# Kernel tuning notes

Hardware: AMD Instinct MI355X
Metric: run time of the kernel (lower is better)

The kernel has to match this reference:

```python
import jax, jax.numpy as jnp
import numpy as np

H, W = 48, 48
L = H * W            # 2304 tokens
D = 256              # d_model
NH = 8               # heads (self and memory attn)
FF = 1024            # dim_feedforward
T = 2                # memory frames
BS = 1
GN_GROUPS = 32       # GNActDWConv2d default groups


def layernorm(x, g, b, eps=1e-5):
    m = jnp.mean(x, -1, keepdims=True)
    v = jnp.mean((x - m) ** 2, -1, keepdims=True)
    return (x - m) * jax.lax.rsqrt(v + eps) * g + b


def linear(x, Wt, b):
    # torch nn.Linear convention: Wt is [out, in]
    return x @ Wt.T + b


def mha_core(Q, K, V, nhead):
    # Q [Lq, bs, C], K/V [Lk, bs, C]; AOT MultiheadAttention core (eval: no dropout)
    Lq, bs, C = Q.shape
    hd = C // nhead
    Qh = (Q / np.float32(np.sqrt(hd))).reshape(Lq, bs, nhead, hd).transpose(1, 2, 0, 3)
    Kh = K.reshape(-1, bs, nhead, hd).transpose(1, 2, 0, 3)
    Vh = V.reshape(-1, bs, nhead, hd).transpose(1, 2, 0, 3)
    attn = jax.nn.softmax(jnp.einsum('bhqd,bhkd->bhqk', Qh, Kh), axis=-1)
    out = jnp.einsum('bhqk,bhkd->bhqd', attn, Vh)
    return out.transpose(2, 0, 1, 3).reshape(Lq, bs, C)


def groupnorm(x, g, b, groups, eps=1e-5):
    bs, c, h, w = x.shape
    xg = x.reshape(bs, groups, c // groups, h, w)
    m = jnp.mean(xg, (2, 3, 4), keepdims=True)
    v = jnp.mean((xg - m) ** 2, (2, 3, 4), keepdims=True)
    xg = (xg - m) * jax.lax.rsqrt(v + eps)
    return xg.reshape(bs, c, h, w) * g[None, :, None, None] + b[None, :, None, None]


def dwconv5(x, k):
    # depthwise 5x5, padding=2; x [bs,c,h,w], k [c,1,5,5]
    return jax.lax.conv_general_dilated(x, k, (1, 1), ((2, 2), (2, 2)),
                                        feature_group_count=x.shape[1])


def setup_inputs() -> dict:
    key = jax.random.key(0)
    ks = jax.random.split(key, 16)
    rn = lambda i, shape, s=1.0: jax.random.normal(ks[i], shape, jnp.float32) * s
    w = 0.02
    inp = {
        'tgt': rn(0, (L, BS, D)),
        'global_K': rn(1, (T, L, BS, D)),
        'global_V': rn(2, (T, L, BS, D)),
        'local_K': rn(3, (L, BS, D)),
        'local_V': rn(4, (L, BS, D)),
        # LayerNorms
        'ln1_g': jnp.ones(D, jnp.float32), 'ln1_b': jnp.zeros(D, jnp.float32),
        'ln2_g': jnp.ones(D, jnp.float32), 'ln2_b': jnp.zeros(D, jnp.float32),
        'ln3_g': jnp.ones(D, jnp.float32), 'ln3_b': jnp.zeros(D, jnp.float32),
        'ln4_g': jnp.ones(D, jnp.float32), 'ln4_b': jnp.zeros(D, jnp.float32),
        # self_attn (use_linear=True) Q/K/V + projection
        'sa_Wq': rn(5, (D, D), w), 'sa_bq': jnp.zeros(D, jnp.float32),
        'sa_Wk': rn(6, (D, D), w), 'sa_bk': jnp.zeros(D, jnp.float32),
        'sa_Wv': rn(7, (D, D), w), 'sa_bv': jnp.zeros(D, jnp.float32),
        'sa_Wo': rn(8, (D, D), w), 'sa_bo': jnp.zeros(D, jnp.float32),
        # block linear_Q
        'Wq': rn(9, (D, D), w), 'bq': jnp.zeros(D, jnp.float32),
        # long/short term attn projections (use_linear=False)
        'lt_Wo': rn(10, (D, D), w), 'lt_bo': jnp.zeros(D, jnp.float32),
        'st_Wo': rn(11, (D, D), w), 'st_bo': jnp.zeros(D, jnp.float32),
        # FFN: linear1 -> GN+GELU+DWConv -> linear2
        'W1': rn(12, (FF, D), w), 'b1': jnp.zeros(FF, jnp.float32),
        'gn_g': jnp.ones(FF, jnp.float32), 'gn_b': jnp.zeros(FF, jnp.float32),
        'dw_k': rn(13, (FF, 1, 5, 5), 0.05),
        'W2': rn(14, (D, FF), w), 'b2': jnp.zeros(D, jnp.float32),
    }
    return inp


def reference(tgt, global_K, global_V, local_K, local_V,
              ln1_g, ln1_b, ln2_g, ln2_b, ln3_g, ln3_b, ln4_g, ln4_b,
              sa_Wq, sa_bq, sa_Wk, sa_bk, sa_Wv, sa_bv, sa_Wo, sa_bo,
              Wq, bq, lt_Wo, lt_bo, st_Wo, st_bo,
              W1, b1, gn_g, gn_b, dw_k, W2, b2):
    # --- stage 1: self-attention ---
    _tgt = layernorm(tgt, ln1_g, ln1_b)
    q = linear(_tgt, sa_Wq, sa_bq)
    k = linear(_tgt, sa_Wk, sa_bk)
    v = linear(_tgt, sa_Wv, sa_bv)
    tgt2 = linear(mha_core(q, k, v, NH), sa_Wo, sa_bo)
    tgt = tgt + tgt2  # droppath is identity at eval

    # --- stage 2: long-term + short-term memory cross-attention ---
    _tgt = layernorm(tgt, ln2_g, ln2_b)
    curr_Q = linear(_tgt, Wq, bq)
    curr_K = curr_Q
    curr_V = _tgt

    flat_K = global_K.reshape(-1, BS, D)  # [T*L, bs, D]
    flat_V = global_V.reshape(-1, BS, D)
    tgt2 = linear(mha_core(curr_Q, flat_K, flat_V, NH), lt_Wo, lt_bo)

    k_st = layernorm(local_K + curr_K, ln4_g, ln4_b)
    v_st = layernorm(local_V + curr_V, ln4_g, ln4_b)
    tgt3 = linear(mha_core(curr_Q, k_st, v_st, NH), st_Wo, st_bo)

    tgt = tgt + tgt2 + tgt3

    # --- stage 3: FFN with GN + GELU + depthwise conv ---
    _tgt = layernorm(tgt, ln3_g, ln3_b)
    x = linear(_tgt, W1, b1)                        # [L, bs, FF]
    x = x.reshape(H, W, BS, FF).transpose(2, 3, 0, 1)  # [bs, FF, H, W]
    x = jax.nn.gelu(groupnorm(x, gn_g, gn_b, GN_GROUPS), approximate=False)
    x = dwconv5(x, dw_k)
    x = x.reshape(BS, FF, L).transpose(2, 0, 1)     # [L, bs, FF]
    tgt2 = linear(x, W2, b2)
    return tgt + tgt2
```

## Files before the change

kernel.cpp:

```cpp
#include <hip/hip_runtime.h>
#include <hip/hip_bf16.h>

#define L   2304
#define D   256
#define NHD 8
#define HD  32
#define FF  1024
#define HH  48
#define WWW 48
#define SPL 4
#define RCH 24
#define RP  (L / RCH)

typedef unsigned short bfraw;
typedef __attribute__((ext_vector_type(8))) short s8v;
typedef __attribute__((ext_vector_type(4))) float f4v;

__device__ __forceinline__ bfraw f2b(float x) {
    __hip_bfloat16 h = __float2bfloat16(x);
    return __builtin_bit_cast(bfraw, h);
}

__global__ __launch_bounds__(256) void diag_kernel(float* __restrict__ out, float c, int n)
{
    int i = blockIdx.x * 256 + threadIdx.x;
    if (i < n) out[i] = c;
}

__global__ __launch_bounds__(256) void ln_kernel(
    const float* __restrict__ inA, const float* __restrict__ inB,
    const float* __restrict__ g, const float* __restrict__ b,
    float* __restrict__ out, bfraw* __restrict__ outb)
{
    int row = blockIdx.x, t = threadIdx.x;
    size_t idx = (size_t)row * D + t;
    float v = inA[idx];
    if (inB) v += inB[idx];
    __shared__ float rs[256], rq[256];
    rs[t] = v; rq[t] = v * v;
    __syncthreads();
    for (int o = 128; o > 0; o >>= 1) {
        if (t < o) { rs[t] += rs[t + o]; rq[t] += rq[t + o]; }
        __syncthreads();
    }
    float mean = rs[0] * (1.f / D);
    float var  = rq[0] * (1.f / D) - mean * mean;
    float rstd = rsqrtf(var + 1e-5f);
    float r = (v - mean) * rstd * g[t] + b[t];
    out[idx] = r;
    if (outb) outb[idx] = f2b(r);
}

__global__ __launch_bounds__(256) void gemm_mfma(
    const float* __restrict__ A, const float* __restrict__ W,
    const float* __restrict__ bias, const float* res, float* out,
    bfraw* __restrict__ outb,
    int M, int N, int K)
{
    __shared__ __attribute__((aligned(16))) short Al[32][32];
    __shared__ __attribute__((aligned(16))) short Wl[64][32];
    int t = threadIdx.x;
    int w = t >> 6, l = t & 63;
    int lo = l & 15, quad = l >> 4;
    int m0 = blockIdx.x * 32, n0 = blockIdx.y * 64;
    int wr = (w & 1) * 16, wc = (w >> 1) * 32;
    f4v acc[2];
    acc[0] = (f4v){0.f, 0.f, 0.f, 0.f};
    acc[1] = (f4v){0.f, 0.f, 0.f, 0.f};

    int aswz = (quad ^ ((lo >> 2) & 3)) * 8;
    int arow = t >> 3, apart = t & 7;
    int acol = ((apart >> 1) ^ ((arow >> 2) & 3)) * 8 + (apart & 1) * 4;

    for (int k0 = 0; k0 < K; k0 += 32) {
        float4 a4 = *reinterpret_cast<const float4*>(A + (size_t)(m0 + arow) * K + k0 + apart * 4);
        float4 w4[2];
        #pragma unroll
        for (int i = 0; i < 2; i++) {
            int row = i * 32 + arow;
            w4[i] = *reinterpret_cast<const float4*>(W + (size_t)(n0 + row) * K + k0 + apart * 4);
        }
        __syncthreads();
        {
            ushort4 ab;
            ab.x = f2b(a4.x); ab.y = f2b(a4.y); ab.z = f2b(a4.z); ab.w = f2b(a4.w);
            *reinterpret_cast<ushort4*>(&Al[arow][acol]) = ab;
            #pragma unroll
            for (int i = 0; i < 2; i++) {
                int row = i * 32 + arow;
                int col = ((apart >> 1) ^ ((row >> 2) & 3)) * 8 + (apart & 1) * 4;
                ushort4 wb;
                wb.x = f2b(w4[i].x); wb.y = f2b(w4[i].y); wb.z = f2b(w4[i].z); wb.w = f2b(w4[i].w);
                *reinterpret_cast<ushort4*>(&Wl[row][col]) = wb;
            }
        }
        __syncthreads();
        s8v af = *reinterpret_cast<const s8v*>(&Al[wr + lo][aswz]);
        #pragma unroll
        for (int j = 0; j < 2; j++) {
            s8v wf = *reinterpret_cast<const s8v*>(&Wl[wc + j * 16 + lo][aswz]);
            acc[j] = __builtin_amdgcn_mfma_f32_16x16x32_bf16(af, wf, acc[j], 0, 0, 0);
        }
    }

    #pragma unroll
    for (int j = 0; j < 2; j++) {
        #pragma unroll
        for (int r = 0; r < 4; r++) {
            int mrow = m0 + wr + quad * 4 + r;
            int ncol = n0 + wc + j * 16 + lo;
            float v = acc[j][r] + bias[ncol];
            size_t idx = (size_t)mrow * N + ncol;
            if (res) v += res[idx];
            out[idx] = v;
            if (outb) outb[idx] = f2b(v);
        }
    }
}

__global__ __launch_bounds__(256) void cvt_kernel(
    const float* __restrict__ in, bfraw* __restrict__ out)
{
    size_t i = ((size_t)blockIdx.x * 256 + threadIdx.x) * 4;
    float4 v = *reinterpret_cast<const float4*>(in + i);
    ushort4 o;
    o.x = f2b(v.x); o.y = f2b(v.y); o.z = f2b(v.z); o.w = f2b(v.w);
    *reinterpret_cast<ushort4*>(out + i) = o;
}

__global__ __launch_bounds__(256) void cvtT_kernel(
    const float* __restrict__ in, bfraw* __restrict__ out, int N)
{
    __shared__ float Ls[32][33];
    int h = blockIdx.y, n0 = blockIdx.x * 32, t = threadIdx.x;
    int nl = t >> 3, dq = t & 7;
    float4 v = *reinterpret_cast<const float4*>(in + (size_t)(n0 + nl) * D + h * HD + dq * 4);
    Ls[nl][dq*4+0] = v.x; Ls[nl][dq*4+1] = v.y;
    Ls[nl][dq*4+2] = v.z; Ls[nl][dq*4+3] = v.w;
    __syncthreads();
    int dl = t >> 3, nq = t & 7;
    ushort4 o;
    o.x = f2b(Ls[nq*4+0][dl]); o.y = f2b(Ls[nq*4+1][dl]);
    o.z = f2b(Ls[nq*4+2][dl]); o.w = f2b(Ls[nq*4+3][dl]);
    *reinterpret_cast<ushort4*>(out + (size_t)(h * HD + dl) * N + n0 + nq * 4) = o;
}

__global__ __launch_bounds__(256) void attn_mfma_split(
    const bfraw* __restrict__ Qb, const bfraw* __restrict__ Kb,
    const bfraw* __restrict__ Vt, float* __restrict__ OP,
    float* __restrict__ ML, int Lk, int chunk, float scale)
{
    __shared__ __attribute__((aligned(16))) short Ks[64][32];
    __shared__ __attribute__((aligned(16))) short Vts[32][72];
    __shared__ __attribute__((aligned(16))) short Ps[4][16][72];
    int t = threadIdx.x;
    int w = t >> 6, l = t & 63;
    int h = blockIdx.y, q0 = blockIdx.x * 64 + w * 16, z = blockIdx.z;
    int lo = l & 15, quad = l >> 4;
    int kb = z * chunk, ke = kb + chunk;

    s8v qf = *reinterpret_cast<const s8v*>(Qb + (size_t)(q0 + lo) * D + h * HD + quad * 8);
    int kswz = (quad ^ ((lo >> 2) & 3)) * 8;

    int skey = t >> 2, spart = t & 3;
    int kcol = (spart ^ ((skey >> 2) & 3)) * 8;
    int sd = t >> 3, svp = t & 7;
    const bfraw* kp = Kb + (size_t)skey * D + h * HD + spart * 8;
    const bfraw* vp = Vt + (size_t)(h * HD + sd) * Lk + svp * 8;

    float m_r = -1e30f, l_r = 0.f;
    f4v o0 = {0.f, 0.f, 0.f, 0.f}, o1 = {0.f, 0.f, 0.f, 0.f};

    for (int k0 = kb; k0 < ke; k0 += 64) {
        s8v kv = *reinterpret_cast<const s8v*>(kp + (size_t)k0 * D);
        s8v vv = *reinterpret_cast<const s8v*>(vp + k0);
        __syncthreads();
        *reinterpret_cast<s8v*>(&Ks[skey][kcol]) = kv;
        *reinterpret_cast<s8v*>(&Vts[sd][svp * 8]) = vv;
        __syncthreads();

        f4v sc4[4];
        #pragma unroll
        for (int s = 0; s < 4; s++) {
            s8v kf = *reinterpret_cast<const s8v*>(&Ks[lo + 16 * s][kswz]);
            sc4[s] = __builtin_amdgcn_mfma_f32_16x16x32_bf16(kf, qf, (f4v){0.f,0.f,0.f,0.f}, 0, 0, 0);
        }
        float cm = -1e30f;
        #pragma unroll
        for (int s = 0; s < 4; s++)
            #pragma unroll
            for (int r = 0; r < 4; r++) {
                sc4[s][r] *= scale;
                cm = fmaxf(cm, sc4[s][r]);
            }
        cm = fmaxf(cm, __shfl_xor(cm, 16));
        cm = fmaxf(cm, __shfl_xor(cm, 32));
        float mnew = fmaxf(m_r, cm);
        float alpha = __expf(m_r - mnew);
        float ls = 0.f;
        #pragma unroll
        for (int s = 0; s < 4; s++) {
            float p0 = __expf(sc4[s][0] - mnew), p1 = __expf(sc4[s][1] - mnew);
            float p2 = __expf(sc4[s][2] - mnew), p3 = __expf(sc4[s][3] - mnew);
            ls += p0 + p1 + p2 + p3;
            ushort4 pk;
            pk.x = f2b(p0); pk.y = f2b(p1); pk.z = f2b(p2); pk.w = f2b(p3);
            *reinterpret_cast<ushort4*>(&Ps[w][lo][s * 16 + quad * 4]) = pk;
        }
        ls += __shfl_xor(ls, 16);
        ls += __shfl_xor(ls, 32);
        l_r = l_r * alpha + ls;
        m_r = mnew;
        #pragma unroll
        for (int r = 0; r < 4; r++) {
            float a = __shfl(alpha, quad * 4 + r);
            o0[r] *= a; o1[r] *= a;
        }
        #pragma unroll
        for (int kc = 0; kc < 2; kc++) {
            s8v pf = *reinterpret_cast<const s8v*>(&Ps[w][lo][kc * 32 + quad * 8]);
            s8v v0 = *reinterpret_cast<const s8v*>(&Vts[lo][kc * 32 + quad * 8]);
            s8v v1 = *reinterpret_cast<const s8v*>(&Vts[16 + lo][kc * 32 + quad * 8]);
            o0 = __builtin_amdgcn_mfma_f32_16x16x32_bf16(pf, v0, o0, 0, 0, 0);
            o1 = __builtin_amdgcn_mfma_f32_16x16x32_bf16(pf, v1, o1, 0, 0, 0);
        }
    }

    float* Oz = OP + (size_t)z * L * D;
    #pragma unroll
    for (int r = 0; r < 4; r++) {
        int qg = q0 + quad * 4 + r;
        Oz[(size_t)qg * D + h * HD + lo]      = o0[r];
        Oz[(size_t)qg * D + h * HD + 16 + lo] = o1[r];
    }
    if (l < 16) {
        size_t mi = (((size_t)z * NHD + h) * L + q0 + lo) * 2;
        ML[mi]     = m_r;
        ML[mi + 1] = l_r;
    }
}

__global__ __launch_bounds__(256) void attn_combine(
    const float* __restrict__ OP, const float* __restrict__ ML,
    float* __restrict__ O)
{
    int q = blockIdx.x, t = threadIdx.x, h = t >> 5;
    float m[SPL], lv[SPL];
    float M = -1e30f;
    #pragma unroll
    for (int s = 0; s < SPL; s++) {
        size_t mi = (((size_t)s * NHD + h) * L + q) * 2;
        m[s]  = ML[mi];
        lv[s] = ML[mi + 1];
        M = fmaxf(M, m[s]);
    }
    float wl = 0.f, acc = 0.f;
    #pragma unroll
    for (int s = 0; s < SPL; s++) {
        float w = __expf(m[s] - M);
        wl  += w * lv[s];
        acc += w * OP[(size_t)s * L * D + (size_t)q * D + t];
    }
    O[(size_t)q * D + t] = acc / wl;
}

__global__ __launch_bounds__(256) void gn_stats_part(
    const float* __restrict__ X, float* __restrict__ ps)
{
    int g = blockIdx.x, rc = blockIdx.y, t = threadIdx.x;
    int cq = (t & 7) * 4;
    int rl = t >> 3;
    int r0 = rc * RP;
    float s = 0.f, sq = 0.f;
    #pragma unroll
    for (int p = 0; p < RP / 32; p++) {
        int l = r0 + p * 32 + rl;
        float4 v = *reinterpret_cast<const float4*>(X + (size_t)l * FF + g * 32 + cq);
        s  += v.x + v.y + v.z + v.w;
        sq += v.x*v.x + v.y*v.y + v.z*v.z + v.w*v.w;
    }
    __shared__ float rs[256], rq[256];
    rs[t] = s; rq[t] = sq;
    __syncthreads();
    for (int o = 128; o > 0; o >>= 1) {
        if (t < o) { rs[t] += rs[t + o]; rq[t] += rq[t + o]; }
        __syncthreads();
    }
    if (t == 0) {
        ps[(g * RCH + rc) * 2]     = rs[0];
        ps[(g * RCH + rc) * 2 + 1] = rq[0];
    }
}

__global__ __launch_bounds__(64) void gn_stats_final(
    const float* __restrict__ ps, float* __restrict__ st)
{
    int g = threadIdx.x;
    if (g < 32) {
        float s = 0.f, sq = 0.f;
        for (int i = 0; i < RCH; i++) {
            s  += ps[(g * RCH + i) * 2];
            sq += ps[(g * RCH + i) * 2 + 1];
        }
        float n = (float)(L * 32);
        float mean = s / n;
        float var  = sq / n - mean * mean;
        st[g * 2]     = mean;
        st[g * 2 + 1] = rsqrtf(var + 1e-5f);
    }
}

__global__ __launch_bounds__(256) void gn_gelu_dwconv(
    const float* __restrict__ X, const float* __restrict__ st,
    const float* __restrict__ gg, const float* __restrict__ gb,
    const float* __restrict__ Kw, float* __restrict__ Y)
{
    __shared__ float tile[144][64];
    int h0 = blockIdx.x * 8, w0 = blockIdx.y * 8, c0 = blockIdx.z * 64;
    int t = threadIdx.x;
    int c = t & 63;
    int cg = (c0 + c) >> 5;
    float mu = st[2 * cg], rs = st[2 * cg + 1];
    float ga = gg[c0 + c], be = gb[c0 + c];

    for (int i = t; i < 144 * 64; i += 256) {
        int sp = i >> 6;
        int hy = h0 + (sp / 12) - 2, wx = w0 + (sp % 12) - 2;
        float v = 0.f;
        if (hy >= 0 && hy < HH && wx >= 0 && wx < WWW) {
            float x = X[(size_t)(hy * WWW + wx) * FF + c0 + c];
            x = (x - mu) * rs * ga + be;
            v = 0.5f * x * (1.f + erff(x * 0.70710678118654752f));
        }
        tile[sp][c] = v;
    }
    float kw[25];
    #pragma unroll
    for (int i = 0; i < 25; i++) kw[i] = Kw[(size_t)(c0 + c) * 25 + i];
    __syncthreads();

    int sgrp = t >> 6;
    for (int s = 0; s < 16; s++) {
        int sp = sgrp * 16 + s;
        int oh = sp >> 3, ow = sp & 7;
        float acc = 0.f;
        #pragma unroll
        for (int ky = 0; ky < 5; ky++)
            #pragma unroll
            for (int kx = 0; kx < 5; kx++)
                acc += tile[(oh + ky) * 12 + ow + kx][c] * kw[ky * 5 + kx];
        Y[(size_t)((h0 + oh) * WWW + w0 + ow) * FF + c0 + c] = acc;
    }
}

extern "C" void kernel_launch(void* const* d_in, const int* in_sizes, int n_in,
                              void* d_out, int out_size, void* d_ws, size_t ws_size,
                              hipStream_t stream)
{
    (void)in_sizes;
    float* out = (float*)d_out;

    if (n_in != 34) {
        diag_kernel<<<(out_size + 255) / 256, 256, 0, stream>>>(out, 2000.f, out_size);
        return;
    }

    const float* tgt    = (const float*)d_in[0];
    const float* gK     = (const float*)d_in[1];
    const float* gV     = (const float*)d_in[2];
    const float* lK     = (const float*)d_in[3];
    const float* lV     = (const float*)d_in[4];
    const float* ln1_g  = (const float*)d_in[5];
    const float* ln1_b  = (const float*)d_in[6];
    const float* ln2_g  = (const float*)d_in[7];
    const float* ln2_b  = (const float*)d_in[8];
    const float* ln3_g  = (const float*)d_in[9];
    const float* ln3_b  = (const float*)d_in[10];
    const float* ln4_g  = (const float*)d_in[11];
    const float* ln4_b  = (const float*)d_in[12];
    const float* sa_Wq  = (const float*)d_in[13];
    const float* sa_bq  = (const float*)d_in[14];
    const float* sa_Wk  = (const float*)d_in[15];
    const float* sa_bk  = (const float*)d_in[16];
    const float* sa_Wv  = (const float*)d_in[17];
    const float* sa_bv  = (const float*)d_in[18];
    const float* sa_Wo  = (const float*)d_in[19];
    const float* sa_bo  = (const float*)d_in[20];
    const float* Wq     = (const float*)d_in[21];
    const float* bq     = (const float*)d_in[22];
    const float* lt_Wo  = (const float*)d_in[23];
    const float* lt_bo  = (const float*)d_in[24];
    const float* st_Wo  = (const float*)d_in[25];
    const float* st_bo  = (const float*)d_in[26];
    const float* W1w    = (const float*)d_in[27];
    const float* b1w    = (const float*)d_in[28];
    const float* gn_g   = (const float*)d_in[29];
    const float* gn_b   = (const float*)d_in[30];
    const float* dw_k   = (const float*)d_in[31];
    const float* W2w    = (const float*)d_in[32];
    const float* b2w    = (const float*)d_in[33];

    const size_t LD = (size_t)L * D;
    const size_t NEED = (6 * LD + (size_t)L * FF + 64) * 4;
    float* ws = (float*)d_ws;
    float* t0 = ws + 0 * LD;
    float* t1 = ws + 1 * LD;
    float* t2 = ws + 2 * LD;
    float* t3 = ws + 3 * LD;
    float* t4 = ws + 4 * LD;
    float* t5 = ws + 5 * LD;
    float* X1 = t0;
    float* X2 = ws + 6 * LD;
    float* ST = X2 + (size_t)L * FF;
    bfraw* qb   = (bfraw*)X2;
    bfraw* kb1  = qb + LD;
    bfraw* vtb1 = qb + 3 * LD;
    bfraw* kb2  = qb + 5 * LD;
    bfraw* vtb2 = qb + 6 * LD;
    float* OP   = ws;
    float* ML   = X2 + (7 * LD) / 2;
    float* PS   = ML;

    if (ws_size < NEED) {
        int wsMiB = (int)(ws_size >> 20); if (wsMiB > 63) wsMiB = 63;
        diag_kernel<<<(out_size + 255) / 256, 256, 0, stream>>>(out, 64.f + (float)wsMiB, out_size);
        return;
    }

    const float scale = 0.17677669529663687f;
    dim3 gDD(L / 32, D / 64);
    dim3 gDF(L / 32, FF / 64);
    dim3 gATS(L / 64, NHD, SPL);
    int  cvtLD  = (int)(LD / 1024);
    dim3 gT1(L / 32, NHD);
    dim3 gT2(2 * L / 32, NHD);
    dim3 gGN(32, RCH);
    dim3 gDW(6, 6, 16);

    ln_kernel<<<L, 256, 0, stream>>>(tgt, nullptr, ln1_g, ln1_b, t0, nullptr);
    gemm_mfma<<<gDD, 256, 0, stream>>>(t0, sa_Wq, sa_bq, nullptr, t1, qb,  L, D, D);
    gemm_mfma<<<gDD, 256, 0, stream>>>(t0, sa_Wk, sa_bk, nullptr, t2, kb2, L, D, D);
    gemm_mfma<<<gDD, 256, 0, stream>>>(t0, sa_Wv, sa_bv, nullptr, t3, nullptr, L, D, D);
    cvtT_kernel<<<gT1, 256, 0, stream>>>(t3, vtb2, L);
    attn_mfma_split<<<gATS, 256, 0, stream>>>(qb, kb2, vtb2, OP, ML, L, L / SPL, scale);
    attn_combine<<<L, 256, 0, stream>>>(OP, ML, t4);
    gemm_mfma<<<gDD, 256, 0, stream>>>(t4, sa_Wo, sa_bo, tgt, t5, nullptr, L, D, D);

    ln_kernel<<<L, 256, 0, stream>>>(t5, nullptr, ln2_g, ln2_b, t0, nullptr);
    gemm_mfma<<<gDD, 256, 0, stream>>>(t0, Wq, bq, nullptr, t1, qb, L, D, D);
    ln_kernel<<<L, 256, 0, stream>>>(t1, lK, ln4_g, ln4_b, t2, kb2);
    ln_kernel<<<L, 256, 0, stream>>>(t0, lV, ln4_g, ln4_b, t3, nullptr);
    cvtT_kernel<<<gT1, 256, 0, stream>>>(t3, vtb2, L);
    cvt_kernel<<<2 * cvtLD, 256, 0, stream>>>(gK, kb1);
    cvtT_kernel<<<gT2, 256, 0, stream>>>(gV, vtb1, 2 * L);
    attn_mfma_split<<<gATS, 256, 0, stream>>>(qb, kb1, vtb1, OP, ML, 2 * L, 2 * L / SPL, scale);
    attn_combine<<<L, 256, 0, stream>>>(OP, ML, t4);
    gemm_mfma<<<gDD, 256, 0, stream>>>(t4, lt_Wo, lt_bo, t5, t5, nullptr, L, D, D);
    attn_mfma_split<<<gATS, 256, 0, stream>>>(qb, kb2, vtb2, OP, ML, L, L / SPL, scale);
    attn_combine<<<L, 256, 0, stream>>>(OP, ML, t4);
    gemm_mfma<<<gDD, 256, 0, stream>>>(t4, st_Wo, st_bo, t5, t5, nullptr, L, D, D);

    ln_kernel<<<L, 256, 0, stream>>>(t5, nullptr, ln3_g, ln3_b, t4, nullptr);
    gemm_mfma<<<gDF, 256, 0, stream>>>(t4, W1w, b1w, nullptr, X1, nullptr, L, FF, D);
    gn_stats_part<<<gGN, 256, 0, stream>>>(X1, PS);
    gn_stats_final<<<1, 64, 0, stream>>>(PS, ST);
    gn_gelu_dwconv<<<gDW, 256, 0, stream>>>(X1, ST, gn_g, gn_b, dw_k, X2);
    gemm_mfma<<<gDD, 256, 0, stream>>>(X2, W2w, b2w, t5, out, nullptr, L, D, FF);
}
```

Before: 363.4 us.

## Fold softmax scale into Q, use exp2 with lazy rescale, transpose PV output

The attention scale times log2(e) is folded into the bf16 Q written by the projection GEMM, so the attention kernel uses exp2 directly and skips the per-score multiply. The running max is only rescaled when any lane's new block max exceeds the old one by more than 8, which removes most alpha rescaling and shuffles. The PV MFMA operands are swapped and the output is staged through LDS to emit coalesced float4 stores. Lazy rescaling bounds growth at 2^8 per block, so there is some fp32 accumulation range risk. The stage-2 Q stays unscaled in fp32 for the K LayerNorm input, so only the bf16 copy carries the scale.

```diff
diff --git a/kernel.cpp b/kernel.cpp
--- a/kernel.cpp
+++ b/kernel.cpp
@@ -11,6 +11,7 @@
 #define SPL 4
 #define RCH 24
 #define RP  (L / RCH)
+#define S2LOG 0.25503486f
 
 typedef unsigned short bfraw;
 typedef __attribute__((ext_vector_type(8))) short s8v;
@@ -54,7 +55,7 @@
 __global__ __launch_bounds__(256) void gemm_mfma(
     const float* __restrict__ A, const float* __restrict__ W,
     const float* __restrict__ bias, const float* res, float* out,
-    bfraw* __restrict__ outb,
+    bfraw* __restrict__ outb, float oscale,
     int M, int N, int K)
 {
     __shared__ __attribute__((aligned(16))) short Al[32][32];
@@ -113,7 +114,7 @@
             size_t idx = (size_t)mrow * N + ncol;
             if (res) v += res[idx];
             out[idx] = v;
-            if (outb) outb[idx] = f2b(v);
+            if (outb) outb[idx] = f2b(v * oscale);
         }
     }
 }
@@ -148,11 +149,12 @@
 __global__ __launch_bounds__(256) void attn_mfma_split(
     const bfraw* __restrict__ Qb, const bfraw* __restrict__ Kb,
     const bfraw* __restrict__ Vt, float* __restrict__ OP,
-    float* __restrict__ ML, int Lk, int chunk, float scale)
+    float* __restrict__ ML, int Lk, int chunk)
 {
     __shared__ __attribute__((aligned(16))) short Ks[64][32];
     __shared__ __attribute__((aligned(16))) short Vts[32][72];
     __shared__ __attribute__((aligned(16))) short Ps[4][16][72];
+    __shared__ float Tb[4][16][33];
     int t = threadIdx.x;
     int w = t >> 6, l = t & 63;
     int h = blockIdx.y, q0 = blockIdx.x * 64 + w * 16, z = blockIdx.z;
@@ -189,19 +191,26 @@
         #pragma unroll
         for (int s = 0; s < 4; s++)
             #pragma unroll
-            for (int r = 0; r < 4; r++) {
-                sc4[s][r] *= scale;
+            for (int r = 0; r < 4; r++)
                 cm = fmaxf(cm, sc4[s][r]);
-            }
         cm = fmaxf(cm, __shfl_xor(cm, 16));
         cm = fmaxf(cm, __shfl_xor(cm, 32));
-        float mnew = fmaxf(m_r, cm);
-        float alpha = __expf(m_r - mnew);
+        bool skip = __all(cm <= m_r + 8.f);
+        if (!skip) {
+            float mnew = fmaxf(m_r, cm);
+            float alpha = __builtin_amdgcn_exp2f(m_r - mnew);
+            l_r *= alpha;
+            #pragma unroll
+            for (int r = 0; r < 4; r++) { o0[r] *= alpha; o1[r] *= alpha; }
+            m_r = mnew;
+        }
         float ls = 0.f;
         #pragma unroll
         for (int s = 0; s < 4; s++) {
-            float p0 = __expf(sc4[s][0] - mnew), p1 = __expf(sc4[s][1] - mnew);
-            float p2 = __expf(sc4[s][2] - mnew), p3 = __expf(sc4[s][3] - mnew);
+            float p0 = __builtin_amdgcn_exp2f(sc4[s][0] - m_r);
+            float p1 = __builtin_amdgcn_exp2f(sc4[s][1] - m_r);
+            float p2 = __builtin_amdgcn_exp2f(sc4[s][2] - m_r);
+            float p3 = __builtin_amdgcn_exp2f(sc4[s][3] - m_r);
             ls += p0 + p1 + p2 + p3;
             ushort4 pk;
             pk.x = f2b(p0); pk.y = f2b(p1); pk.z = f2b(p2); pk.w = f2b(p3);
@@ -209,30 +218,31 @@
         }
         ls += __shfl_xor(ls, 16);
         ls += __shfl_xor(ls, 32);
-        l_r = l_r * alpha + ls;
-        m_r = mnew;
-        #pragma unroll
-        for (int r = 0; r < 4; r++) {
-            float a = __shfl(alpha, quad * 4 + r);
-            o0[r] *= a; o1[r] *= a;
-        }
+        l_r += ls;
         #pragma unroll
         for (int kc = 0; kc < 2; kc++) {
             s8v pf = *reinterpret_cast<const s8v*>(&Ps[w][lo][kc * 32 + quad * 8]);
             s8v v0 = *reinterpret_cast<const s8v*>(&Vts[lo][kc * 32 + quad * 8]);
             s8v v1 = *reinterpret_cast<const s8v*>(&Vts[16 + lo][kc * 32 + quad * 8]);
-            o0 = __builtin_amdgcn_mfma_f32_16x16x32_bf16(pf, v0, o0, 0, 0, 0);
-            o1 = __builtin_amdgcn_mfma_f32_16x16x32_bf16(pf, v1, o1, 0, 0, 0);
-        }
-    }
-
+            o0 = __builtin_amdgcn_mfma_f32_16x16x32_bf16(v0, pf, o0, 0, 0, 0);
+            o1 = __builtin_amdgcn_mfma_f32_16x16x32_bf16(v1, pf, o1, 0, 0, 0);
+        }
+    }
+
+    #pragma unroll
+    for (int r = 0; r < 4; r++) {
+        Tb[w][lo][quad * 4 + r]      = o0[r];
+        Tb[w][lo][16 + quad * 4 + r] = o1[r];
+    }
     float* Oz = OP + (size_t)z * L * D;
-    #pragma unroll
-    for (int r = 0; r < 4; r++) {
-        int qg = q0 + quad * 4 + r;
-        Oz[(size_t)qg * D + h * HD + lo]      = o0[r];
-        Oz[(size_t)qg * D + h * HD + 16 + lo] = o1[r];
-    }
+    int ql = l >> 2, dq = (l & 3) * 8;
+    float4 u0, u1;
+    u0.x = Tb[w][ql][dq + 0]; u0.y = Tb[w][ql][dq + 1];
+    u0.z = Tb[w][ql][dq + 2]; u0.w = Tb[w][ql][dq + 3];
+    u1.x = Tb[w][ql][dq + 4]; u1.y = Tb[w][ql][dq + 5];
+    u1.z = Tb[w][ql][dq + 6]; u1.w = Tb[w][ql][dq + 7];
+    *reinterpret_cast<float4*>(Oz + (size_t)(q0 + ql) * D + h * HD + dq)     = u0;
+    *reinterpret_cast<float4*>(Oz + (size_t)(q0 + ql) * D + h * HD + dq + 4) = u1;
     if (l < 16) {
         size_t mi = (((size_t)z * NHD + h) * L + q0 + lo) * 2;
         ML[mi]     = m_r;
@@ -257,7 +267,7 @@
     float wl = 0.f, acc = 0.f;
     #pragma unroll
     for (int s = 0; s < SPL; s++) {
-        float w = __expf(m[s] - M);
+        float w = __builtin_amdgcn_exp2f(m[s] - M);
         wl  += w * lv[s];
         acc += w * OP[(size_t)s * L * D + (size_t)q * D + t];
     }
@@ -427,7 +437,6 @@
         return;
     }
 
-    const float scale = 0.17677669529663687f;
     dim3 gDD(L / 32, D / 64);
     dim3 gDF(L / 32, FF / 64);
     dim3 gATS(L / 64, NHD, SPL);
@@ -438,32 +447,32 @@
     dim3 gDW(6, 6, 16);
 
     ln_kernel<<<L, 256, 0, stream>>>(tgt, nullptr, ln1_g, ln1_b, t0, nullptr);
-    gemm_mfma<<<gDD, 256, 0, stream>>>(t0, sa_Wq, sa_bq, nullptr, t1, qb,  L, D, D);
-    gemm_mfma<<<gDD, 256, 0, stream>>>(t0, sa_Wk, sa_bk, nullptr, t2, kb2, L, D, D);
-    gemm_mfma<<<gDD, 256, 0, stream>>>(t0, sa_Wv, sa_bv, nullptr, t3, nullptr, L, D, D);
+    gemm_mfma<<<gDD, 256, 0, stream>>>(t0, sa_Wq, sa_bq, nullptr, t1, qb,  S2LOG, L, D, D);
+    gemm_mfma<<<gDD, 256, 0, stream>>>(t0, sa_Wk, sa_bk, nullptr, t2, kb2, 1.f,   L, D, D);
+    gemm_mfma<<<gDD, 256, 0, stream>>>(t0, sa_Wv, sa_bv, nullptr, t3, nullptr, 1.f, L, D, D);
     cvtT_kernel<<<gT1, 256, 0, stream>>>(t3, vtb2, L);
-    attn_mfma_split<<<gATS, 256, 0, stream>>>(qb, kb2, vtb2, OP, ML, L, L / SPL, scale);
+    attn_mfma_split<<<gATS, 256, 0, stream>>>(qb, kb2, vtb2, OP, ML, L, L / SPL);
     attn_combine<<<L, 256, 0, stream>>>(OP, ML, t4);
-    gemm_mfma<<<gDD, 256, 0, stream>>>(t4, sa_Wo, sa_bo, tgt, t5, nullptr, L, D, D);
+    gemm_mfma<<<gDD, 256, 0, stream>>>(t4, sa_Wo, sa_bo, tgt, t5, nullptr, 1.f, L, D, D);
 
     ln_kernel<<<L, 256, 0, stream>>>(t5, nullptr, ln2_g, ln2_b, t0, nullptr);
-    gemm_mfma<<<gDD, 256, 0, stream>>>(t0, Wq, bq, nullptr, t1, qb, L, D, D);
+    gemm_mfma<<<gDD, 256, 0, stream>>>(t0, Wq, bq, nullptr, t1, qb, S2LOG, L, D, D);
     ln_kernel<<<L, 256, 0, stream>>>(t1, lK, ln4_g, ln4_b, t2, kb2);
     ln_kernel<<<L, 256, 0, stream>>>(t0, lV, ln4_g, ln4_b, t3, nullptr);
     cvtT_kernel<<<gT1, 256, 0, stream>>>(t3, vtb2, L);
     cvt_kernel<<<2 * cvtLD, 256, 0, stream>>>(gK, kb1);
     cvtT_kernel<<<gT2, 256, 0, stream>>>(gV, vtb1, 2 * L);
-    attn_mfma_split<<<gATS, 256, 0, stream>>>(qb, kb1, vtb1, OP, ML, 2 * L, 2 * L / SPL, scale);
+    attn_mfma_split<<<gATS, 256, 0, stream>>>(qb, kb1, vtb1, OP, ML, 2 * L, 2 * L / SPL);
     attn_combine<<<L, 256, 0, stream>>>(OP, ML, t4);
-    gemm_mfma<<<gDD, 256, 0, stream>>>(t4, lt_Wo, lt_bo, t5, t5, nullptr, L, D, D);
-    attn_mfma_split<<<gATS, 256, 0, stream>>>(qb, kb2, vtb2, OP, ML, L, L / SPL, scale);
+    gemm_mfma<<<gDD, 256, 0, stream>>>(t4, lt_Wo, lt_bo, t5, t5, nullptr, 1.f, L, D, D);
+    attn_mfma_split<<<gATS, 256, 0, stream>>>(qb, kb2, vtb2, OP, ML, L, L / SPL);
     attn_combine<<<L, 256, 0, stream>>>(OP, ML, t4);
-    gemm_mfma<<<gDD, 256, 0, stream>>>(t4, st_Wo, st_bo, t5, t5, nullptr, L, D, D);
+    gemm_mfma<<<gDD, 256, 0, stream>>>(t4, st_Wo, st_bo, t5, t5, nullptr, 1.f, L, D, D);
 
     ln_kernel<<<L, 256, 0, stream>>>(t5, nullptr, ln3_g, ln3_b, t4, nullptr);
-    gemm_mfma<<<gDF, 256, 0, stream>>>(t4, W1w, b1w, nullptr, X1, nullptr, L, FF, D);
+    gemm_mfma<<<gDF, 256, 0, stream>>>(t4, W1w, b1w, nullptr, X1, nullptr, 1.f, L, FF, D);
     gn_stats_part<<<gGN, 256, 0, stream>>>(X1, PS);
     gn_stats_final<<<1, 64, 0, stream>>>(PS, ST);
     gn_gelu_dwconv<<<gDW, 256, 0, stream>>>(X1, ST, gn_g, gn_b, dw_k, X2);
-    gemm_mfma<<<gDD, 256, 0, stream>>>(X2, W2w, b2w, t5, out, nullptr, L, D, FF);
-}
+    gemm_mfma<<<gDD, 256, 0, stream>>>(X2, W2w, b2w, t5, out, nullptr, 1.f, L, D, FF);
+}
```

Result: faster. 348.3 us (-4.2%).
